# Kernel optimization log

Hardware: AMD Instinct MI355X
Metric: run time of the kernel (lower is better)

## Reference

```python
import jax, jax.numpy as jnp
import numpy as np

E, K = 8, 2          # num_experts, top_k
D, I = 1024, 2048    # hidden_dim, intermediate_dim
B, S = 4, 1024       # batch, seq_len


def setup_inputs() -> dict:
    key = jax.random.key(0)
    k0, k1, k2, k3, k4 = jax.random.split(key, 5)
    hidden_states = jax.random.normal(k0, (B, S, D), dtype=jnp.float32)
    Wc = jax.random.normal(k1, (E, D), dtype=jnp.float32) * (1.0 / np.sqrt(D))
    bc = jnp.zeros((E,), dtype=jnp.float32)
    Wg = jax.random.normal(k2, (E, D, I), dtype=jnp.float32) * (1.0 / np.sqrt(D))
    Wu = jax.random.normal(k3, (E, D, I), dtype=jnp.float32) * (1.0 / np.sqrt(D))
    Wd = jax.random.normal(k4, (E, I, D), dtype=jnp.float32) * (1.0 / np.sqrt(I))
    return {"hidden_states": hidden_states, "Wc": Wc, "bc": bc,
            "Wg": Wg, "Wu": Wu, "Wd": Wd}


def reference(hidden_states, Wc, bc, Wg, Wu, Wd):
    b, s, d = hidden_states.shape
    x = hidden_states.reshape(-1, d)                       # [T, D]
    # Confidence heads: one scalar per (token, expert), sigmoid-activated.
    conf = jax.nn.sigmoid(jnp.einsum('td,ed->te', x, Wc) + bc)  # [T, E]
    # Auction routing: top_k by confidence, softmax over selected bids.
    top_vals, top_idx = jax.lax.top_k(conf, K)             # [T, K]
    rweights = jax.nn.softmax(top_vals, axis=-1)           # [T, K]
    # Combine weights per (token, expert): sum_k rw_k * one_hot(idx_k).
    comb = jnp.sum(jax.nn.one_hot(top_idx, E, dtype=x.dtype)
                   * rweights[..., None], axis=1)          # [T, E]
    # SwiGLU experts (dense compute over all experts, sparse combine).
    g = jnp.einsum('td,edi->tei', x, Wg)                   # [T, E, I]
    u = jnp.einsum('td,edi->tei', x, Wu)                   # [T, E, I]
    h = jax.nn.silu(g) * u                                 # [T, E, I]
    y = jnp.einsum('tei,eid->ted', h, Wd)                  # [T, E, D]
    out = jnp.einsum('ted,te->td', y, comb)                # [T, D]
    return out.reshape(b, s, d)
```

## Files before the change

### kernel.cpp

```cpp
#include <hip/hip_runtime.h>

#define T_TOK 4096
#define DDIM  1024
#define IDIM  2048
#define NE    8
#define TOTROWS 8192

typedef unsigned short u16;
typedef unsigned int   u32;
typedef _Float16 f16;
typedef _Float16 f16x8 __attribute__((ext_vector_type(8)));
typedef _Float16 f16x4 __attribute__((ext_vector_type(4)));
typedef float    f32x4 __attribute__((ext_vector_type(4)));

static __device__ __forceinline__ void gload16(const f16* g, f16* l) {
  __builtin_amdgcn_global_load_lds(
      (const __attribute__((address_space(1))) void*)g,
      (__attribute__((address_space(3))) void*)l, 16, 0, 0);
}

__global__ __launch_bounds__(256) void conf_kernel(
    const float* __restrict__ x, const float* __restrict__ Wc,
    const float* __restrict__ bc, float* __restrict__ conf)
{
  int gid  = blockIdx.x * 256 + threadIdx.x;
  int t    = gid >> 6;
  int lane = threadIdx.x & 63;
  if (t >= T_TOK) return;
  const float* xr = x + (size_t)t * DDIM;
  float acc[NE];
#pragma unroll
  for (int e = 0; e < NE; e++) acc[e] = 0.f;
  for (int d = lane; d < DDIM; d += 64) {
    float xv = xr[d];
#pragma unroll
    for (int e = 0; e < NE; e++) acc[e] += xv * Wc[e * DDIM + d];
  }
#pragma unroll
  for (int off = 32; off > 0; off >>= 1) {
#pragma unroll
    for (int e = 0; e < NE; e++) acc[e] += __shfl_down(acc[e], off, 64);
  }
  if (lane == 0) {
#pragma unroll
    for (int e = 0; e < NE; e++)
      conf[t * NE + e] = 1.f / (1.f + expf(-(acc[e] + bc[e])));
  }
}

__global__ __launch_bounds__(256) void top2_kernel(
    const float* __restrict__ conf,
    int* __restrict__ counts, int* __restrict__ list, float* __restrict__ wlist)
{
  int t = blockIdx.x * 256 + threadIdx.x;
  if (t >= T_TOK) return;
  float c[NE];
#pragma unroll
  for (int e = 0; e < NE; e++) c[e] = conf[t * NE + e];
  int i0 = 0;
#pragma unroll
  for (int e = 1; e < NE; e++) if (c[e] > c[i0]) i0 = e;
  int i1 = (i0 == 0) ? 1 : 0;
#pragma unroll
  for (int e = 0; e < NE; e++) if (e != i0 && c[e] > c[i1]) i1 = e;
  float w1 = 1.f / (1.f + expf(c[i0] - c[i1]));
  float w0 = 1.f - w1;
  int s0 = atomicAdd(&counts[i0], 1);
  list[i0 * T_TOK + s0]  = t;
  wlist[i0 * T_TOK + s0] = w0;
  int s1 = atomicAdd(&counts[i1], 1);
  list[i1 * T_TOK + s1]  = t;
  wlist[i1 * T_TOK + s1] = w1;
}

__global__ void scan_kernel(const int* __restrict__ counts, int* __restrict__ base)
{
  if (threadIdx.x == 0 && blockIdx.x == 0) {
    int s = 0;
    for (int e = 0; e < NE; e++) { base[e] = s; s += counts[e]; }
    base[NE] = s;
  }
}

__global__ __launch_bounds__(256) void cvt_x_kernel(
    const float* __restrict__ x, f16* __restrict__ xh)
{
  int i = blockIdx.x * 256 + threadIdx.x;
  float4 v = ((const float4*)x)[i];
  f16x4 h; h[0] = (f16)v.x; h[1] = (f16)v.y; h[2] = (f16)v.z; h[3] = (f16)v.w;
  ((f16x4*)xh)[i] = h;
}

__global__ __launch_bounds__(256) void tpose_kernel(
    const float* __restrict__ in, f16* __restrict__ out, int R, int C)
{
  __shared__ float t[32][33];
  const size_t mat = (size_t)R * C;
  const float* src = in  + (size_t)blockIdx.z * mat;
  f16*         dst = out + (size_t)blockIdx.z * mat;
  int c0 = blockIdx.x * 32, r0 = blockIdx.y * 32;
  int tx = threadIdx.x & 31, ty = threadIdx.x >> 5;
#pragma unroll
  for (int i = 0; i < 32; i += 8)
    t[ty + i][tx] = src[(size_t)(r0 + ty + i) * C + c0 + tx];
  __syncthreads();
#pragma unroll
  for (int i = 0; i < 32; i += 8)
    dst[(size_t)(c0 + ty + i) * R + r0 + tx] = (f16)t[tx][ty + i];
}

constexpr int BK = 32;

__global__ __launch_bounds__(256, 2) void gemm1_kernel(
    const f16* __restrict__ xh, const f16* __restrict__ WgT, const f16* __restrict__ WuT,
    const int* __restrict__ counts, const int* __restrict__ base,
    const int* __restrict__ list, const float* __restrict__ wlist,
    f16* __restrict__ hbuf)
{
  const int e   = blockIdx.z;
  const int cnt = counts[e];
  const int p0  = blockIdx.y * 128;
  if (p0 >= cnt) return;
  const int n0  = blockIdx.x * 128;

  __shared__ __align__(16) f16 As [2][128 * BK];
  __shared__ __align__(16) f16 Bgs[2][128 * BK];
  __shared__ __align__(16) f16 Bus[2][128 * BK];
  __shared__ int   tokS[128];
  __shared__ float wS[128];

  const int tid = threadIdx.x;
  if (tid < 128) {
    int p = p0 + tid;
    tokS[tid] = (p < cnt) ? list[e * T_TOK + p] : 0;
    wS[tid]   = (p < cnt) ? wlist[e * T_TOK + p] : 0.f;
  }
  __syncthreads();

  const int l   = tid & 63;
  const int w   = tid >> 6;
  const int wr  = w >> 1, wc = w & 1;
  const int r15 = l & 15;
  const int kg  = l >> 4;

  const int rl4 = l >> 2;
  const int sl  = (l & 3) ^ ((l >> 3) & 3);
  const f16* WgE = WgT + ((size_t)e << 21);
  const f16* WuE = WuT + ((size_t)e << 21);
  const f16* srcA[2]; const f16* srcG[2]; const f16* srcU[2];
#pragma unroll
  for (int ii = 0; ii < 2; ii++) {
    int j = 2 * w + ii;
    int row = j * 16 + rl4;
    srcA[ii] = xh  + (size_t)tokS[row] * DDIM + sl * 8;
    srcG[ii] = WgE + (size_t)(n0 + row) * DDIM + sl * 8;
    srcU[ii] = WuE + (size_t)(n0 + row) * DDIM + sl * 8;
  }

  const int phys = kg ^ ((r15 >> 1) & 3);
  const int aoff = (wr * 64 + r15) * BK + phys * 8;
  const int boff = (wc * 64 + r15) * BK + phys * 8;

  f32x4 accg[4][4], accu[4][4];
#pragma unroll
  for (int a = 0; a < 4; a++)
#pragma unroll
    for (int bq = 0; bq < 4; bq++)
#pragma unroll
      for (int r = 0; r < 4; r++) { accg[a][bq][r] = 0.f; accu[a][bq][r] = 0.f; }

#define STAGE1(KT, B) do {                                   \
    int koff = (KT) * BK;                                    \
    _Pragma("unroll")                                        \
    for (int ii = 0; ii < 2; ii++) {                         \
      int j = 2 * w + ii;                                    \
      gload16(srcA[ii] + koff, &As [B][j * 512]);            \
      gload16(srcG[ii] + koff, &Bgs[B][j * 512]);            \
      gload16(srcU[ii] + koff, &Bus[B][j * 512]);            \
    }                                                        \
  } while (0)

  STAGE1(0, 0);
  constexpr int NT = DDIM / BK;
  for (int kt = 0; kt < NT; kt++) {
    const int b = kt & 1;
    __syncthreads();
    if (kt + 1 < NT) STAGE1(kt + 1, b ^ 1);

    f16x8 av[4], bgv[4], buv[4];
#pragma unroll
    for (int mi = 0; mi < 4; mi++) av[mi] = *(const f16x8*)&As[b][aoff + mi * 512];
#pragma unroll
    for (int ni = 0; ni < 4; ni++) {
      bgv[ni] = *(const f16x8*)&Bgs[b][boff + ni * 512];
      buv[ni] = *(const f16x8*)&Bus[b][boff + ni * 512];
    }
#pragma unroll
    for (int mi = 0; mi < 4; mi++)
#pragma unroll
      for (int ni = 0; ni < 4; ni++) {
        accg[mi][ni] = __builtin_amdgcn_mfma_f32_16x16x32_f16(av[mi], bgv[ni], accg[mi][ni], 0, 0, 0);
        accu[mi][ni] = __builtin_amdgcn_mfma_f32_16x16x32_f16(av[mi], buv[ni], accu[mi][ni], 0, 0, 0);
      }
  }
#undef STAGE1

  const int rowbase = base[e] + p0;
#pragma unroll
  for (int mi = 0; mi < 4; mi++)
#pragma unroll
    for (int ni = 0; ni < 4; ni++) {
      int col = n0 + wc * 64 + ni * 16 + r15;
#pragma unroll
      for (int r = 0; r < 4; r++) {
        int p = wr * 64 + mi * 16 + kg * 4 + r;
        if (p0 + p < cnt) {
          float g = accg[mi][ni][r], u = accu[mi][ni][r];
          hbuf[(size_t)(rowbase + p) * IDIM + col] = (f16)(g / (1.f + expf(-g)) * u * wS[p]);
        }
      }
    }
}

__global__ __launch_bounds__(256, 2) void gemm2_kernel(
    const f16* __restrict__ hbuf, const f16* __restrict__ WdT,
    const int* __restrict__ counts, const int* __restrict__ base,
    const int* __restrict__ list, float* __restrict__ out)
{
  const int e   = blockIdx.z;
  const int cnt = counts[e];
  const int p0  = blockIdx.y * 128;
  if (p0 >= cnt) return;
  const int n0  = blockIdx.x * 128;

  __shared__ __align__(16) f16 Hs [2][128 * BK];
  __shared__ __align__(16) f16 Bds[2][128 * BK];
  __shared__ int tokS[128];

  const int tid = threadIdx.x;
  if (tid < 128) {
    int p = p0 + tid;
    tokS[tid] = (p < cnt) ? list[e * T_TOK + p] : 0;
  }
  __syncthreads();

  const int l   = tid & 63;
  const int w   = tid >> 6;
  const int wr  = w >> 1, wc = w & 1;
  const int r15 = l & 15;
  const int kg  = l >> 4;

  const int rl4 = l >> 2;
  const int sl  = (l & 3) ^ ((l >> 3) & 3);
  const int rowbase = base[e] + p0;
  const f16* WdE = WdT + ((size_t)e << 21);
  const f16* srcH[2]; const f16* srcD[2];
#pragma unroll
  for (int ii = 0; ii < 2; ii++) {
    int j = 2 * w + ii;
    int row = j * 16 + rl4;
    int hr = rowbase + row; if (hr > TOTROWS - 1) hr = TOTROWS - 1;
    srcH[ii] = hbuf + (size_t)hr * IDIM + sl * 8;
    srcD[ii] = WdE  + (size_t)(n0 + row) * IDIM + sl * 8;
  }

  const int phys = kg ^ ((r15 >> 1) & 3);
  const int aoff = (wr * 64 + r15) * BK + phys * 8;
  const int boff = (wc * 64 + r15) * BK + phys * 8;

  f32x4 acc[4][4];
#pragma unroll
  for (int a = 0; a < 4; a++)
#pragma unroll
    for (int bq = 0; bq < 4; bq++)
#pragma unroll
      for (int r = 0; r < 4; r++) acc[a][bq][r] = 0.f;

#define STAGE2(KT, B) do {                                   \
    int koff = (KT) * BK;                                    \
    _Pragma("unroll")                                        \
    for (int ii = 0; ii < 2; ii++) {                         \
      int j = 2 * w + ii;                                    \
      gload16(srcH[ii] + koff, &Hs [B][j * 512]);            \
      gload16(srcD[ii] + koff, &Bds[B][j * 512]);            \
    }                                                        \
  } while (0)

  STAGE2(0, 0);
  constexpr int NT = IDIM / BK;
  for (int kt = 0; kt < NT; kt++) {
    const int b = kt & 1;
    __syncthreads();
    if (kt + 1 < NT) STAGE2(kt + 1, b ^ 1);

    f16x8 av[4], bdv[4];
#pragma unroll
    for (int mi = 0; mi < 4; mi++) av[mi] = *(const f16x8*)&Hs[b][aoff + mi * 512];
#pragma unroll
    for (int ni = 0; ni < 4; ni++) bdv[ni] = *(const f16x8*)&Bds[b][boff + ni * 512];
#pragma unroll
    for (int mi = 0; mi < 4; mi++)
#pragma unroll
      for (int ni = 0; ni < 4; ni++)
        acc[mi][ni] = __builtin_amdgcn_mfma_f32_16x16x32_f16(av[mi], bdv[ni], acc[mi][ni], 0, 0, 0);
  }
#undef STAGE2

#pragma unroll
  for (int mi = 0; mi < 4; mi++)
#pragma unroll
    for (int ni = 0; ni < 4; ni++) {
      int col = n0 + wc * 64 + ni * 16 + r15;
#pragma unroll
      for (int r = 0; r < 4; r++) {
        int p = wr * 64 + mi * 16 + kg * 4 + r;
        if (p0 + p < cnt)
          atomicAdd(&out[(size_t)tokS[p] * DDIM + col], acc[mi][ni][r]);
      }
    }
}

extern "C" void kernel_launch(void* const* d_in, const int* in_sizes, int n_in,
                              void* d_out, int out_size, void* d_ws, size_t ws_size,
                              hipStream_t stream)
{
  const float* x  = (const float*)d_in[0];
  const float* Wc = (const float*)d_in[1];
  const float* bc = (const float*)d_in[2];
  const float* Wg = (const float*)d_in[3];
  const float* Wu = (const float*)d_in[4];
  const float* Wd = (const float*)d_in[5];
  float* out = (float*)d_out;

  char* ws = (char*)d_ws;
  int*   counts = (int*)(ws + 0);
  int*   base   = (int*)(ws + 256);
  float* conf   = (float*)(ws + 1024);
  int*   list   = (int*)(ws + 132096);
  float* wlist  = (float*)(ws + 263168);
  f16*   xh     = (f16*)(ws + 394240);
  f16*   hbuf   = (f16*)(ws + 8782848);
  f16*   W1     = (f16*)(ws + 42337280);
  f16*   W2     = (f16*)(ws + 75891712);

  hipMemsetAsync(counts, 0, 64, stream);
  hipMemsetAsync(out, 0, (size_t)out_size * sizeof(float), stream);

  conf_kernel<<<T_TOK / 4, 256, 0, stream>>>(x, Wc, bc, conf);
  top2_kernel<<<T_TOK / 256, 256, 0, stream>>>(conf, counts, list, wlist);
  scan_kernel<<<1, 64, 0, stream>>>(counts, base);

  cvt_x_kernel<<<T_TOK * DDIM / 1024, 256, 0, stream>>>(x, xh);
  dim3 gt1(IDIM / 32, DDIM / 32, NE);
  tpose_kernel<<<gt1, 256, 0, stream>>>(Wg, W1, DDIM, IDIM);
  tpose_kernel<<<gt1, 256, 0, stream>>>(Wu, W2, DDIM, IDIM);

  dim3 g1(IDIM / 128, T_TOK / 128, NE);
  gemm1_kernel<<<g1, 256, 0, stream>>>(xh, W1, W2, counts, base, list, wlist, hbuf);

  dim3 gt2(DDIM / 32, IDIM / 32, NE);
  tpose_kernel<<<gt2, 256, 0, stream>>>(Wd, W1, IDIM, DDIM);

  dim3 g2(DDIM / 128, T_TOK / 128, NE);
  gemm2_kernel<<<g2, 256, 0, stream>>>(hbuf, W1, counts, base, list, out);
}
```

Before: 499.4 us.

## Triple-buffer LDS tiles with explicit vmcnt waits in both expert GEMMs

Both expert GEMM kernels move from double to triple buffering in LDS, prefetching two k-tiles ahead. Each iteration waits with an explicit s_waitcnt vmcnt and a raw s_barrier instead of __syncthreads, so global-to-LDS loads for later tiles can stay in flight while the current tile is computed. The MFMA block is wrapped in s_setprio, and gemm2's launch bound asks for three blocks per CU. This raises LDS use and depends on the vmcnt counts being correct. It also relies on the barrier placement to keep the buffer about to be overwritten from still being read.

Result: faster. 468.5 us (-6.2%).

```diff
diff --git a/kernel.cpp b/kernel.cpp
--- a/kernel.cpp
+++ b/kernel.cpp
@@ -12,6 +12,8 @@
 typedef _Float16 f16x8 __attribute__((ext_vector_type(8)));
 typedef _Float16 f16x4 __attribute__((ext_vector_type(4)));
 typedef float    f32x4 __attribute__((ext_vector_type(4)));
+
+#define WAITV(N) asm volatile("s_waitcnt vmcnt(" #N ")" ::: "memory")
 
 static __device__ __forceinline__ void gload16(const f16* g, f16* l) {
   __builtin_amdgcn_global_load_lds(
@@ -123,9 +125,9 @@
   if (p0 >= cnt) return;
   const int n0  = blockIdx.x * 128;
 
-  __shared__ __align__(16) f16 As [2][128 * BK];
-  __shared__ __align__(16) f16 Bgs[2][128 * BK];
-  __shared__ __align__(16) f16 Bus[2][128 * BK];
+  __shared__ __align__(16) f16 As [3][128 * BK];
+  __shared__ __align__(16) f16 Bgs[3][128 * BK];
+  __shared__ __align__(16) f16 Bus[3][128 * BK];
   __shared__ int   tokS[128];
   __shared__ float wS[128];
 
@@ -181,20 +183,26 @@
   } while (0)
 
   STAGE1(0, 0);
+  STAGE1(1, 1);
   constexpr int NT = DDIM / BK;
+  int cb = 0;
   for (int kt = 0; kt < NT; kt++) {
-    const int b = kt & 1;
-    __syncthreads();
-    if (kt + 1 < NT) STAGE1(kt + 1, b ^ 1);
+    if (kt + 1 < NT) { WAITV(6); } else { WAITV(0); }
+    __builtin_amdgcn_s_barrier();
+    if (kt + 2 < NT) {
+      int sb = (cb == 0) ? 2 : cb - 1;
+      STAGE1(kt + 2, sb);
+    }
 
     f16x8 av[4], bgv[4], buv[4];
 #pragma unroll
-    for (int mi = 0; mi < 4; mi++) av[mi] = *(const f16x8*)&As[b][aoff + mi * 512];
+    for (int mi = 0; mi < 4; mi++) av[mi] = *(const f16x8*)&As[cb][aoff + mi * 512];
 #pragma unroll
     for (int ni = 0; ni < 4; ni++) {
-      bgv[ni] = *(const f16x8*)&Bgs[b][boff + ni * 512];
-      buv[ni] = *(const f16x8*)&Bus[b][boff + ni * 512];
-    }
+      bgv[ni] = *(const f16x8*)&Bgs[cb][boff + ni * 512];
+      buv[ni] = *(const f16x8*)&Bus[cb][boff + ni * 512];
+    }
+    __builtin_amdgcn_s_setprio(1);
 #pragma unroll
     for (int mi = 0; mi < 4; mi++)
 #pragma unroll
@@ -202,6 +210,8 @@
         accg[mi][ni] = __builtin_amdgcn_mfma_f32_16x16x32_f16(av[mi], bgv[ni], accg[mi][ni], 0, 0, 0);
         accu[mi][ni] = __builtin_amdgcn_mfma_f32_16x16x32_f16(av[mi], buv[ni], accu[mi][ni], 0, 0, 0);
       }
+    __builtin_amdgcn_s_setprio(0);
+    cb = (cb == 2) ? 0 : cb + 1;
   }
 #undef STAGE1
 
@@ -222,7 +232,7 @@
     }
 }
 
-__global__ __launch_bounds__(256, 2) void gemm2_kernel(
+__global__ __launch_bounds__(256, 3) void gemm2_kernel(
     const f16* __restrict__ hbuf, const f16* __restrict__ WdT,
     const int* __restrict__ counts, const int* __restrict__ base,
     const int* __restrict__ list, float* __restrict__ out)
@@ -233,8 +243,8 @@
   if (p0 >= cnt) return;
   const int n0  = blockIdx.x * 128;
 
-  __shared__ __align__(16) f16 Hs [2][128 * BK];
-  __shared__ __align__(16) f16 Bds[2][128 * BK];
+  __shared__ __align__(16) f16 Hs [3][128 * BK];
+  __shared__ __align__(16) f16 Bds[3][128 * BK];
   __shared__ int tokS[128];
 
   const int tid = threadIdx.x;
@@ -287,22 +297,30 @@
   } while (0)
 
   STAGE2(0, 0);
+  STAGE2(1, 1);
   constexpr int NT = IDIM / BK;
+  int cb = 0;
   for (int kt = 0; kt < NT; kt++) {
-    const int b = kt & 1;
-    __syncthreads();
-    if (kt + 1 < NT) STAGE2(kt + 1, b ^ 1);
+    if (kt + 1 < NT) { WAITV(4); } else { WAITV(0); }
+    __builtin_amdgcn_s_barrier();
+    if (kt + 2 < NT) {
+      int sb = (cb == 0) ? 2 : cb - 1;
+      STAGE2(kt + 2, sb);
+    }
 
     f16x8 av[4], bdv[4];
 #pragma unroll
-    for (int mi = 0; mi < 4; mi++) av[mi] = *(const f16x8*)&Hs[b][aoff + mi * 512];
-#pragma unroll
-    for (int ni = 0; ni < 4; ni++) bdv[ni] = *(const f16x8*)&Bds[b][boff + ni * 512];
+    for (int mi = 0; mi < 4; mi++) av[mi] = *(const f16x8*)&Hs[cb][aoff + mi * 512];
+#pragma unroll
+    for (int ni = 0; ni < 4; ni++) bdv[ni] = *(const f16x8*)&Bds[cb][boff + ni * 512];
+    __builtin_amdgcn_s_setprio(1);
 #pragma unroll
     for (int mi = 0; mi < 4; mi++)
 #pragma unroll
       for (int ni = 0; ni < 4; ni++)
         acc[mi][ni] = __builtin_amdgcn_mfma_f32_16x16x32_f16(av[mi], bdv[ni], acc[mi][ni], 0, 0, 0);
+    __builtin_amdgcn_s_setprio(0);
+    cb = (cb == 2) ? 0 : cb + 1;
   }
 #undef STAGE2
 
```
